# Kernel optimization log

Measured on AMD Instinct MI355X. Metric: run time of the kernel, lower is better.

## Reference

```python
import jax, jax.numpy as jnp
import numpy as np

N_NODES = 20000
N_EDGES = 320000
IN_CH = 256
HID_CH = 256   # 2 * out_channels
OUT_CH = 128


def gcn_conv(x, edge_index, W, b, n_nodes):
    """PyG GCNConv: linear transform, add self-loops, sym-normalized scatter-add."""
    x = x @ W  # [N, C_out]
    loop = jnp.arange(n_nodes, dtype=edge_index.dtype)
    row = jnp.concatenate([edge_index[0], loop])  # source nodes
    col = jnp.concatenate([edge_index[1], loop])  # destination nodes
    deg = jax.ops.segment_sum(jnp.ones_like(col, dtype=x.dtype), col,
                              num_segments=n_nodes)
    deg_inv_sqrt = jnp.where(deg > 0, jax.lax.rsqrt(deg), 0.0)
    norm = deg_inv_sqrt[row] * deg_inv_sqrt[col]  # [E+N]
    msg = x[row] * norm[:, None]                  # gather + scale
    out = jax.ops.segment_sum(msg, col, num_segments=n_nodes)  # scatter-add
    return out + b


def setup_inputs() -> dict:
    key = jax.random.key(0)
    k1, k2, k3, k4, k5 = jax.random.split(key, 5)
    doc_embeds = jax.random.normal(k1, (N_NODES, IN_CH), dtype=jnp.float32)
    edge_index = jax.random.randint(k2, (2, N_EDGES), 0, N_NODES, dtype=jnp.int64)
    # Glorot-style init for GCN weights, zero bias (PyG defaults)
    s1 = 1.0 / np.sqrt(IN_CH)
    s2 = 1.0 / np.sqrt(HID_CH)
    W1 = jax.random.uniform(k3, (IN_CH, HID_CH), jnp.float32, -s1, s1)
    b1 = jnp.zeros((HID_CH,), jnp.float32)
    W2 = jax.random.uniform(k4, (HID_CH, OUT_CH), jnp.float32, -s2, s2)
    b2 = jnp.zeros((OUT_CH,), jnp.float32)
    return {"doc_embeds": doc_embeds, "edge_index": edge_index,
            "W1": W1, "b1": b1, "W2": W2, "b2": b2}


def reference(doc_embeds, edge_index, W1, b1, W2, b2):
    n = doc_embeds.shape[0]
    x = jax.nn.relu(gcn_conv(doc_embeds, edge_index, W1, b1, n))
    x = gcn_conv(x, edge_index, W2, b2, n)
    return x
```

## Files before the change

### kernel.cpp

```cpp
#include <hip/hip_runtime.h>
#include <math.h>

#define N_NODES 20000
#define N_EDGES 320000
#define IN_CH   256
#define HID_CH  256
#define OUT_CH  128
#define CAP     64

typedef __attribute__((ext_vector_type(8))) short short8;
typedef __attribute__((ext_vector_type(8))) unsigned short ushort8;
typedef __attribute__((ext_vector_type(4))) unsigned short ushort4v;
typedef __attribute__((ext_vector_type(4))) float floatx4;

static __device__ __forceinline__ unsigned short f2bf(float f) {
    unsigned int u = __float_as_uint(f);
    u += 0x7FFFu + ((u >> 16) & 1u);
    return (unsigned short)(u >> 16);
}
static __device__ __forceinline__ float bf2f(unsigned short h) {
    return __uint_as_float(((unsigned int)h) << 16);
}

__global__ __launch_bounds__(256)
void init_kernel(const float* __restrict__ W1, const float* __restrict__ W2,
                 unsigned short* __restrict__ W1thi, unsigned short* __restrict__ W1tlo,
                 unsigned short* __restrict__ W2thi, unsigned short* __restrict__ W2tlo,
                 int* __restrict__ deg) {
    const int g = blockIdx.x * blockDim.x + threadIdx.x;
    const int gsz = gridDim.x * blockDim.x;
    for (int i = g; i < N_NODES; i += gsz) deg[i] = 0;
    for (int i = g; i < IN_CH * HID_CH; i += gsz) {
        int k = i / HID_CH, n = i % HID_CH;
        float x = W1[i];
        unsigned short h = f2bf(x);
        unsigned short l = f2bf(x - bf2f(h));
        W1thi[(size_t)n * IN_CH + k] = h;
        W1tlo[(size_t)n * IN_CH + k] = l;
    }
    for (int i = g; i < HID_CH * OUT_CH; i += gsz) {
        int k = i / OUT_CH, n = i % OUT_CH;
        float x = W2[i];
        unsigned short h = f2bf(x);
        unsigned short l = f2bf(x - bf2f(h));
        W2thi[(size_t)n * HID_CH + k] = h;
        W2tlo[(size_t)n * HID_CH + k] = l;
    }
}

__global__ void degfill_kernel(const int* __restrict__ row, const int* __restrict__ col,
                               int* __restrict__ deg, int* __restrict__ srcs, int E) {
    int i = blockIdx.x * blockDim.x + threadIdx.x;
    if (i < E) {
        int c = col[i];
        int r = row[i];
        int p = atomicAdd(&deg[c], 1);
        srcs[(size_t)c * CAP + p] = r;
    }
}

#define GK 256
template <int AFP32, int TM>
__global__ __launch_bounds__(256)
void gemm_mfma_kernel(const float* __restrict__ Afp,
                      const unsigned short* __restrict__ Ahi, const unsigned short* __restrict__ Alo,
                      const unsigned short* __restrict__ Bthi, const unsigned short* __restrict__ Btlo,
                      const int* __restrict__ deg, float* __restrict__ C, int M, int N) {
    constexpr int MI = TM / 32;
    __shared__ unsigned short As[2][TM][36];
    __shared__ unsigned short Bs[2][128][36];
    const int tid = threadIdx.x;
    const int m0 = blockIdx.y * TM;
    const int n0 = blockIdx.x * 128;
    const int lane = tid & 63;
    const int wave = tid >> 6;
    const int wr = (wave >> 1) * (TM / 2);
    const int wc = (wave & 1) * 64;
    const int lm = lane & 15;
    const int lk = (lane >> 4) * 8;

    floatx4 acc[MI][4];
#pragma unroll
    for (int i = 0; i < MI; ++i)
#pragma unroll
        for (int j = 0; j < 4; ++j) acc[i][j] = (floatx4){0.f, 0.f, 0.f, 0.f};

    for (int k0 = 0; k0 < GK; k0 += 32) {
#pragma unroll
        for (int c = 0; c < TM / 64; ++c) {
            int ch = tid + c * 256;
            int r = ch >> 2;
            int ko = (ch & 3) * 8;
            ushort8 vh = {}, vl = {};
            if (m0 + r < M) {
                if (AFP32) {
                    const float* ap = Afp + (size_t)(m0 + r) * GK + k0 + ko;
                    float4 f0 = *(const float4*)ap;
                    float4 f1 = *(const float4*)(ap + 4);
                    float xs[8] = {f0.x, f0.y, f0.z, f0.w, f1.x, f1.y, f1.z, f1.w};
#pragma unroll
                    for (int j = 0; j < 8; ++j) {
                        vh[j] = f2bf(xs[j]);
                        vl[j] = f2bf(xs[j] - bf2f(vh[j]));
                    }
                } else {
                    size_t ga = (size_t)(m0 + r) * GK + k0 + ko;
                    vh = *(const ushort8*)(Ahi + ga);
                    vl = *(const ushort8*)(Alo + ga);
                }
            }
            *(ushort8*)&As[0][r][ko] = vh;
            *(ushort8*)&As[1][r][ko] = vl;
        }
#pragma unroll
        for (int c = 0; c < 2; ++c) {
            int ch = tid + c * 256;
            int r = ch >> 2;
            int ko = (ch & 3) * 8;
            size_t gb = (size_t)(n0 + r) * GK + k0 + ko;
            *(ushort8*)&Bs[0][r][ko] = *(const ushort8*)(Bthi + gb);
            *(ushort8*)&Bs[1][r][ko] = *(const ushort8*)(Btlo + gb);
        }
        __syncthreads();

        short8 ah[MI], al[MI], bh[4], bl[4];
#pragma unroll
        for (int i = 0; i < MI; ++i) {
            ah[i] = *(const short8*)&As[0][wr + i * 16 + lm][lk];
            al[i] = *(const short8*)&As[1][wr + i * 16 + lm][lk];
        }
#pragma unroll
        for (int j = 0; j < 4; ++j) {
            bh[j] = *(const short8*)&Bs[0][wc + j * 16 + lm][lk];
            bl[j] = *(const short8*)&Bs[1][wc + j * 16 + lm][lk];
        }
#pragma unroll
        for (int i = 0; i < MI; ++i)
#pragma unroll
            for (int j = 0; j < 4; ++j) {
                acc[i][j] = __builtin_amdgcn_mfma_f32_16x16x32_bf16(ah[i], bh[j], acc[i][j], 0, 0, 0);
                acc[i][j] = __builtin_amdgcn_mfma_f32_16x16x32_bf16(ah[i], bl[j], acc[i][j], 0, 0, 0);
                acc[i][j] = __builtin_amdgcn_mfma_f32_16x16x32_bf16(al[i], bh[j], acc[i][j], 0, 0, 0);
            }
        __syncthreads();
    }

#pragma unroll
    for (int i = 0; i < MI; ++i) {
#pragma unroll
        for (int r = 0; r < 4; ++r) {
            int rowi = m0 + wr + i * 16 + (lane >> 4) * 4 + r;
            if (rowi < M) {
                float dr = 1.0f / sqrtf((float)(deg[rowi] + 1));
#pragma unroll
                for (int j = 0; j < 4; ++j) {
                    C[(size_t)rowi * N + n0 + wc + j * 16 + lm] = dr * acc[i][j][r];
                }
            }
        }
    }
}

template <int C, int NSLICE, int MODE>
__global__ __launch_bounds__(256)
void gather_sliced_kernel(const float* __restrict__ X, const int* __restrict__ deg,
                          const int* __restrict__ srcs,
                          const float* __restrict__ bias, float* __restrict__ outf,
                          unsigned short* __restrict__ outhi, unsigned short* __restrict__ outlo,
                          int n) {
    const int slice = blockIdx.x % NSLICE;
    const int ngrp  = blockIdx.x / NSLICE;
    const int wave = threadIdx.x >> 6;
    const int lane = threadIdx.x & 63;
    const int g  = lane >> 3;
    const int sl = lane & 7;
    const int node = ngrp * 32 + wave * 8 + g;
    if (node >= n) return;
    const int choff = slice * 32 + sl * 4;
    const int beg = node * CAP;
    const int cnt = deg[node];

    float4 acc = make_float4(0.f, 0.f, 0.f, 0.f);
    int e = 0;
    for (; e + 4 <= cnt; e += 4) {
        int r0 = srcs[beg + e + 0], r1 = srcs[beg + e + 1];
        int r2 = srcs[beg + e + 2], r3 = srcs[beg + e + 3];
        float4 v0 = *(const float4*)(X + (size_t)r0 * C + choff);
        float4 v1 = *(const float4*)(X + (size_t)r1 * C + choff);
        float4 v2 = *(const float4*)(X + (size_t)r2 * C + choff);
        float4 v3 = *(const float4*)(X + (size_t)r3 * C + choff);
        acc.x += v0.x + v1.x + v2.x + v3.x;
        acc.y += v0.y + v1.y + v2.y + v3.y;
        acc.z += v0.z + v1.z + v2.z + v3.z;
        acc.w += v0.w + v1.w + v2.w + v3.w;
    }
    for (; e < cnt; ++e) {
        int r = srcs[beg + e];
        float4 v = *(const float4*)(X + (size_t)r * C + choff);
        acc.x += v.x; acc.y += v.y; acc.z += v.z; acc.w += v.w;
    }

    const float dc = 1.0f / sqrtf((float)(cnt + 1));
    float4 vs = *(const float4*)(X + (size_t)node * C + choff);
    float4 bb = *(const float4*)(bias + choff);

    float o0 = dc * (acc.x + vs.x) + bb.x;
    float o1 = dc * (acc.y + vs.y) + bb.y;
    float o2 = dc * (acc.z + vs.z) + bb.z;
    float o3 = dc * (acc.w + vs.w) + bb.w;

    if constexpr (MODE == 1) {
        o0 = fmaxf(o0, 0.f); o1 = fmaxf(o1, 0.f);
        o2 = fmaxf(o2, 0.f); o3 = fmaxf(o3, 0.f);
        ushort4v h, l;
        h.x = f2bf(o0); l.x = f2bf(o0 - bf2f(h.x));
        h.y = f2bf(o1); l.y = f2bf(o1 - bf2f(h.y));
        h.z = f2bf(o2); l.z = f2bf(o2 - bf2f(h.z));
        h.w = f2bf(o3); l.w = f2bf(o3 - bf2f(h.w));
        *(ushort4v*)(outhi + (size_t)node * C + choff) = h;
        *(ushort4v*)(outlo + (size_t)node * C + choff) = l;
    } else {
        *(float4*)(outf + (size_t)node * C + choff) = make_float4(o0, o1, o2, o3);
    }
}

extern "C" void kernel_launch(void* const* d_in, const int* in_sizes, int n_in,
                              void* d_out, int out_size, void* d_ws, size_t ws_size,
                              hipStream_t stream) {
    const float* doc_embeds = (const float*)d_in[0];
    const int*   edge_index = (const int*)d_in[1];
    const float* W1 = (const float*)d_in[2];
    const float* b1 = (const float*)d_in[3];
    const float* W2 = (const float*)d_in[4];
    const float* b2 = (const float*)d_in[5];
    float* out = (float*)d_out;

    const int* row = edge_index;
    const int* col = edge_index + N_EDGES;

    char* ws = (char*)d_ws;
    auto align_up = [](size_t x) { return (x + 255) / 256 * 256; };

    float*          X1s  = (float*)(ws);
    unsigned short* H1hi = (unsigned short*)(ws + align_up((size_t)N_NODES * HID_CH * 4));
    unsigned short* H1lo = H1hi + (size_t)N_NODES * HID_CH;
    float*          X2s  = X1s;
    char* meta = (char*)(H1lo + (size_t)N_NODES * HID_CH);
    unsigned short* W1thi = (unsigned short*)(meta); meta += align_up((size_t)IN_CH * HID_CH * 2);
    unsigned short* W1tlo = (unsigned short*)(meta); meta += align_up((size_t)IN_CH * HID_CH * 2);
    unsigned short* W2thi = (unsigned short*)(meta); meta += align_up((size_t)HID_CH * OUT_CH * 2);
    unsigned short* W2tlo = (unsigned short*)(meta); meta += align_up((size_t)HID_CH * OUT_CH * 2);
    int*   deg  = (int*)(meta);  meta += align_up((size_t)N_NODES * 4);
    int*   srcs = (int*)(meta);

    init_kernel<<<256, 256, 0, stream>>>(W1, W2, W1thi, W1tlo, W2thi, W2tlo, deg);
    degfill_kernel<<<(N_EDGES + 255) / 256, 256, 0, stream>>>(row, col, deg, srcs, N_EDGES);

    {
        dim3 grid(HID_CH / 128, (N_NODES + 63) / 64);
        gemm_mfma_kernel<1, 64><<<grid, 256, 0, stream>>>(
            doc_embeds, nullptr, nullptr, W1thi, W1tlo, deg, X1s, N_NODES, HID_CH);
    }
    gather_sliced_kernel<HID_CH, 8, 1><<<((N_NODES + 31) / 32) * 8, 256, 0, stream>>>(
        X1s, deg, srcs, b1, nullptr, H1hi, H1lo, N_NODES);

    {
        dim3 grid(OUT_CH / 128, (N_NODES + 63) / 64);
        gemm_mfma_kernel<0, 64><<<grid, 256, 0, stream>>>(
            nullptr, H1hi, H1lo, W2thi, W2tlo, deg, X2s, N_NODES, OUT_CH);
    }
    gather_sliced_kernel<OUT_CH, 4, 0><<<((N_NODES + 31) / 32) * 4, 256, 0, stream>>>(
        X2s, deg, srcs, b2, out, nullptr, nullptr, N_NODES);
}
```

Measured before the change: 180.1 us.

## Store edge sources as 16-bit indices, vector-load them, and use nontemporal stores

```diff
diff --git a/kernel.cpp b/kernel.cpp
--- a/kernel.cpp
+++ b/kernel.cpp
@@ -49,13 +49,13 @@
 }
 
 __global__ void degfill_kernel(const int* __restrict__ row, const int* __restrict__ col,
-                               int* __restrict__ deg, int* __restrict__ srcs, int E) {
+                               int* __restrict__ deg, unsigned short* __restrict__ srcs, int E) {
     int i = blockIdx.x * blockDim.x + threadIdx.x;
     if (i < E) {
         int c = col[i];
         int r = row[i];
         int p = atomicAdd(&deg[c], 1);
-        srcs[(size_t)c * CAP + p] = r;
+        srcs[(size_t)c * CAP + p] = (unsigned short)r;
     }
 }
 
@@ -164,31 +164,33 @@
 template <int C, int NSLICE, int MODE>
 __global__ __launch_bounds__(256)
 void gather_sliced_kernel(const float* __restrict__ X, const int* __restrict__ deg,
-                          const int* __restrict__ srcs,
+                          const unsigned short* __restrict__ srcs,
                           const float* __restrict__ bias, float* __restrict__ outf,
                           unsigned short* __restrict__ outhi, unsigned short* __restrict__ outlo,
                           int n) {
+    constexpr int SW  = C / NSLICE;
+    constexpr int L   = SW / 4;
+    constexpr int NPW = 64 / L;
     const int slice = blockIdx.x % NSLICE;
     const int ngrp  = blockIdx.x / NSLICE;
     const int wave = threadIdx.x >> 6;
     const int lane = threadIdx.x & 63;
-    const int g  = lane >> 3;
-    const int sl = lane & 7;
-    const int node = ngrp * 32 + wave * 8 + g;
+    const int g  = lane / L;
+    const int sl = lane % L;
+    const int node = ngrp * (4 * NPW) + wave * NPW + g;
     if (node >= n) return;
-    const int choff = slice * 32 + sl * 4;
-    const int beg = node * CAP;
+    const int choff = slice * SW + sl * 4;
+    const size_t beg = (size_t)node * CAP;
     const int cnt = deg[node];
 
     float4 acc = make_float4(0.f, 0.f, 0.f, 0.f);
     int e = 0;
     for (; e + 4 <= cnt; e += 4) {
-        int r0 = srcs[beg + e + 0], r1 = srcs[beg + e + 1];
-        int r2 = srcs[beg + e + 2], r3 = srcs[beg + e + 3];
-        float4 v0 = *(const float4*)(X + (size_t)r0 * C + choff);
-        float4 v1 = *(const float4*)(X + (size_t)r1 * C + choff);
-        float4 v2 = *(const float4*)(X + (size_t)r2 * C + choff);
-        float4 v3 = *(const float4*)(X + (size_t)r3 * C + choff);
+        ushort4v s4 = *(const ushort4v*)(srcs + beg + e);
+        float4 v0 = *(const float4*)(X + (size_t)s4.x * C + choff);
+        float4 v1 = *(const float4*)(X + (size_t)s4.y * C + choff);
+        float4 v2 = *(const float4*)(X + (size_t)s4.z * C + choff);
+        float4 v3 = *(const float4*)(X + (size_t)s4.w * C + choff);
         acc.x += v0.x + v1.x + v2.x + v3.x;
         acc.y += v0.y + v1.y + v2.y + v3.y;
         acc.z += v0.z + v1.z + v2.z + v3.z;
@@ -217,10 +219,11 @@
         h.y = f2bf(o1); l.y = f2bf(o1 - bf2f(h.y));
         h.z = f2bf(o2); l.z = f2bf(o2 - bf2f(h.z));
         h.w = f2bf(o3); l.w = f2bf(o3 - bf2f(h.w));
-        *(ushort4v*)(outhi + (size_t)node * C + choff) = h;
-        *(ushort4v*)(outlo + (size_t)node * C + choff) = l;
+        __builtin_nontemporal_store(h, (ushort4v*)(outhi + (size_t)node * C + choff));
+        __builtin_nontemporal_store(l, (ushort4v*)(outlo + (size_t)node * C + choff));
     } else {
-        *(float4*)(outf + (size_t)node * C + choff) = make_float4(o0, o1, o2, o3);
+        floatx4 o = {o0, o1, o2, o3};
+        __builtin_nontemporal_store(o, (floatx4*)(outf + (size_t)node * C + choff));
     }
 }
 
@@ -250,8 +253,8 @@
     unsigned short* W1tlo = (unsigned short*)(meta); meta += align_up((size_t)IN_CH * HID_CH * 2);
     unsigned short* W2thi = (unsigned short*)(meta); meta += align_up((size_t)HID_CH * OUT_CH * 2);
     unsigned short* W2tlo = (unsigned short*)(meta); meta += align_up((size_t)HID_CH * OUT_CH * 2);
-    int*   deg  = (int*)(meta);  meta += align_up((size_t)N_NODES * 4);
-    int*   srcs = (int*)(meta);
+    int*            deg   = (int*)(meta);            meta += align_up((size_t)N_NODES * 4);
+    unsigned short* srcs  = (unsigned short*)(meta);
 
     init_kernel<<<256, 256, 0, stream>>>(W1, W2, W1thi, W1tlo, W2thi, W2tlo, deg);
     degfill_kernel<<<(N_EDGES + 255) / 256, 256, 0, stream>>>(row, col, deg, srcs, N_EDGES);
@@ -269,6 +272,6 @@
         gemm_mfma_kernel<0, 64><<<grid, 256, 0, stream>>>(
             nullptr, H1hi, H1lo, W2thi, W2tlo, deg, X2s, N_NODES, OUT_CH);
     }
-    gather_sliced_kernel<OUT_CH, 4, 0><<<((N_NODES + 31) / 32) * 4, 256, 0, stream>>>(
+    gather_sliced_kernel<OUT_CH, 8, 0><<<((N_NODES + 63) / 64) * 8, 256, 0, stream>>>(
         X2s, deg, srcs, b2, out, nullptr, nullptr, N_NODES);
 }
```

Measured after the change: 184.3 us. 2.3% more time.
